# Kernel tuning notes

Measured on AMD Instinct MI355X. Metric: run time of the kernel, lower is better.

Reference implementation:

```python
import jax, jax.numpy as jnp
import numpy as np

N_NODES = 50000
N_EDGES = 800000
IN_FEATS, HIDDEN_FEATS, NUM_CLASSES = 64, 64, 32


def setup_inputs() -> dict:
    key = jax.random.key(0)
    ks = jax.random.split(key, 9)
    features = jax.random.normal(ks[0], (N_NODES, IN_FEATS), dtype=jnp.float32)
    src = jax.random.randint(ks[1], (N_EDGES,), 0, N_NODES, dtype=jnp.int32)
    dst = jax.random.randint(ks[2], (N_EDGES,), 0, N_NODES, dtype=jnp.int32)
    def lin(k, fan_in, fan_out):
        bound = 1.0 / np.sqrt(fan_in)
        return jax.random.uniform(k, (fan_in, fan_out), jnp.float32, -bound, bound)
    W_self1 = lin(ks[3], IN_FEATS, HIDDEN_FEATS)
    W_neigh1 = lin(ks[4], IN_FEATS, HIDDEN_FEATS)
    b1 = jnp.zeros((HIDDEN_FEATS,), jnp.float32)
    W_self2 = lin(ks[5], HIDDEN_FEATS, NUM_CLASSES)
    W_neigh2 = lin(ks[6], HIDDEN_FEATS, NUM_CLASSES)
    b2 = jnp.zeros((NUM_CLASSES,), jnp.float32)
    return {"features": features, "W_self1": W_self1, "W_neigh1": W_neigh1, "b1": b1,
            "W_self2": W_self2, "W_neigh2": W_neigh2, "b2": b2, "src": src, "dst": dst}


def _sage_mean(x, W_self, W_neigh, b, src, dst, n_nodes):
    # mean over in-neighbors: edge (u, v) sends x[u] into v
    agg = jax.ops.segment_sum(x[src], dst, num_segments=n_nodes)          # [N, F]
    deg = jax.ops.segment_sum(jnp.ones((src.shape[0],), x.dtype), dst,
                              num_segments=n_nodes)                        # [N]
    h_neigh = agg / jnp.maximum(deg, 1.0)[:, None]                         # zero-in-degree -> 0
    return x @ W_self + h_neigh @ W_neigh + b


def reference(features, W_self1, W_neigh1, b1, W_self2, W_neigh2, b2, src, dst):
    n = features.shape[0]
    h = jax.nn.relu(_sage_mean(features, W_self1, W_neigh1, b1, src, dst, n))
    return _sage_mean(h, W_self2, W_neigh2, b2, src, dst, n)
```

## Files before the change

### kernel.cpp

```cpp
#include <hip/hip_runtime.h>

#define N_NODES 50000
#define N_EDGES 800000
#define NB 196
#define PBLOCKS 256
#define CHUNK 3125
#define GEMM_BLOCKS 782
#define CSR_CAP 4608
#define HST 80

typedef unsigned short ushort_t;
typedef __attribute__((ext_vector_type(8))) short bf16x8;
typedef __attribute__((ext_vector_type(4))) float f32x4;


__device__ __forceinline__ float bflo(unsigned int u) {
    return __uint_as_float(u << 16);
}
__device__ __forceinline__ float bfhi(unsigned int u) {
    return __uint_as_float(u & 0xffff0000u);
}
__device__ __forceinline__ ushort_t f2bf(float f) {
    unsigned int x = __float_as_uint(f);
    return (ushort_t)((x + 0x7fffu + ((x >> 16) & 1u)) >> 16);
}
__device__ __forceinline__ unsigned int pack_bf(float lo, float hi) {
    return (unsigned int)f2bf(lo) | ((unsigned int)f2bf(hi) << 16);
}
__device__ __forceinline__ void split_bf(float v, short& hi, short& lo) {
    ushort_t h = f2bf(v);
    float r = v - __uint_as_float((unsigned int)h << 16);
    hi = (short)h;
    lo = (short)f2bf(r);
}

__global__ __launch_bounds__(256)
void gemm128_and_count(const float* __restrict__ A,
                       const float* __restrict__ B1,
                       const float* __restrict__ B2,
                       ushort_t* __restrict__ Cself,
                       ushort_t* __restrict__ Cn,
                       const int* __restrict__ dst,
                       int* __restrict__ blocktot) {
    __shared__ int hist[NB];

    if (blockIdx.x >= GEMM_BLOCKS) {
        const int pb = blockIdx.x - GEMM_BLOCKS;
        for (int i = threadIdx.x; i < NB; i += 256) hist[i] = 0;
        __syncthreads();
        const int e0 = pb * CHUNK;
        const int e1 = e0 + CHUNK;
        for (int e = e0 + (int)threadIdx.x; e < e1; e += 256)
            atomicAdd(&hist[dst[e] >> 8], 1);
        __syncthreads();
        for (int i = threadIdx.x; i < NB; i += 256)
            blocktot[i * PBLOCKS + pb] = hist[i];
        return;
    }

    const int l  = threadIdx.x & 63;
    const int w  = threadIdx.x >> 6;
    const int lr = l & 15;
    const int lk = (l >> 4) << 3;

    bf16x8 bhi[2][2], blo[2][2];
#pragma unroll
    for (int nt = 0; nt < 2; ++nt) {
        const int n = w * 32 + nt * 16 + lr;
        const float* Bp = (n < 64) ? (B1 + n) : (B2 + (n - 64));
#pragma unroll
        for (int ks = 0; ks < 2; ++ks) {
#pragma unroll
            for (int j = 0; j < 8; ++j) {
                float bv = Bp[(size_t)(ks * 32 + lk + j) * 64];
                short h, lo;
                split_bf(bv, h, lo);
                bhi[nt][ks][j] = h;
                blo[nt][ks][j] = lo;
            }
        }
    }

    const int m0 = blockIdx.x * 64;
    f32x4 acc[4][2];
#pragma unroll
    for (int mt = 0; mt < 4; ++mt)
#pragma unroll
        for (int nt = 0; nt < 2; ++nt) {
            f32x4 z = {0.f, 0.f, 0.f, 0.f};
            acc[mt][nt] = z;
        }

#pragma unroll
    for (int mt = 0; mt < 4; ++mt) {
        const int m = m0 + mt * 16 + lr;
        const bool valid = (m < N_NODES);
        const float* Ap = A + (size_t)m * 64 + lk;
#pragma unroll
        for (int ks = 0; ks < 2; ++ks) {
            float4 f0, f1;
            if (valid) {
                f0 = *(const float4*)(Ap + ks * 32);
                f1 = *(const float4*)(Ap + ks * 32 + 4);
            } else {
                f0 = make_float4(0.f, 0.f, 0.f, 0.f);
                f1 = f0;
            }
            const float fv[8] = {f0.x, f0.y, f0.z, f0.w, f1.x, f1.y, f1.z, f1.w};
            bf16x8 ahi, alo;
#pragma unroll
            for (int j = 0; j < 8; ++j) {
                short h, lo;
                split_bf(fv[j], h, lo);
                ahi[j] = h;
                alo[j] = lo;
            }
#pragma unroll
            for (int nt = 0; nt < 2; ++nt) {
                acc[mt][nt] = __builtin_amdgcn_mfma_f32_16x16x32_bf16(
                    ahi, bhi[nt][ks], acc[mt][nt], 0, 0, 0);
                acc[mt][nt] = __builtin_amdgcn_mfma_f32_16x16x32_bf16(
                    alo, bhi[nt][ks], acc[mt][nt], 0, 0, 0);
                acc[mt][nt] = __builtin_amdgcn_mfma_f32_16x16x32_bf16(
                    ahi, blo[nt][ks], acc[mt][nt], 0, 0, 0);
            }
        }
    }

#pragma unroll
    for (int mt = 0; mt < 4; ++mt) {
        const int mbase = m0 + mt * 16 + ((l >> 4) << 2);
#pragma unroll
        for (int nt = 0; nt < 2; ++nt) {
            const int n = w * 32 + nt * 16 + lr;
            ushort_t* T = (n < 64) ? (Cself + n) : (Cn + (n - 64));
#pragma unroll
            for (int r = 0; r < 4; ++r) {
                const int m = mbase + r;
                if (m < N_NODES) T[(size_t)m * 64] = f2bf(acc[mt][nt][r]);
            }
        }
    }
}

__global__ __launch_bounds__(256)
void part_write(const int* __restrict__ src, const int* __restrict__ dst,
                const int* __restrict__ blocktot, unsigned int* __restrict__ brec) {
    __shared__ int ssum[256];
    __shared__ int cur[NB];
    const int pb = blockIdx.x;
    const int t  = threadIdx.x;

    int rsum = 0, mypart = 0;
    if (t < NB) {
        const int* rp = blocktot + t * PBLOCKS;
#pragma unroll 8
        for (int j = 0; j < PBLOCKS; ++j) {
            if (j == pb) mypart = rsum;
            rsum += rp[j];
        }
    }
    ssum[t] = (t < NB) ? rsum : 0;
    __syncthreads();
    for (int off = 1; off < 256; off <<= 1) {
        int add = (t >= off) ? ssum[t - off] : 0;
        __syncthreads();
        ssum[t] += add;
        __syncthreads();
    }
    if (t < NB) cur[t] = (ssum[t] - rsum) + mypart;
    __syncthreads();

    const int e0 = pb * CHUNK;
    const int e1 = e0 + CHUNK;
    for (int e = e0 + t; e < e1; e += 256) {
        int d = dst[e];
        int s = src[e];
        int pos = atomicAdd(&cur[d >> 8], 1);
        brec[pos] = ((unsigned int)(d & 255) << 16) | (unsigned int)s;
    }
}

__global__ __launch_bounds__(1024)
void csr_gather1_g2(const int* __restrict__ blocktot,
                    const unsigned int* __restrict__ brec,
                    int* __restrict__ csr_src, int* __restrict__ row_ptr,
                    const ushort_t* __restrict__ Tself,
                    const ushort_t* __restrict__ Tn,
                    const float* __restrict__ bias,
                    const float* __restrict__ Ws2,
                    const float* __restrict__ Wn2,
                    ushort_t* __restrict__ Tself2,
                    ushort_t* __restrict__ Tn2) {
    __shared__ int ssum[256];
    __shared__ int cnt[256];
    __shared__ int rs[256];
    __shared__ int cur[256];
    __shared__ int csr_lds[CSR_CAP];
    __shared__ ushort_t h_lds[256 * HST];

    const int b = blockIdx.x;
    const int node0 = b * 256;
    const int t = threadIdx.x;

    {
        unsigned int* hz = (unsigned int*)h_lds;
        for (int i = t; i < 256 * HST / 2; i += 1024) hz[i] = 0u;
    }

    if (t < 256) {
        int rsum = 0;
        if (t < NB) {
            const int* rp = blocktot + t * PBLOCKS;
#pragma unroll 8
            for (int j = 0; j < PBLOCKS; ++j) rsum += rp[j];
        }
        ssum[t] = rsum;
        cnt[t] = 0;
    }
    __syncthreads();
    for (int off = 1; off < 256; off <<= 1) {
        int add = (t < 256 && t >= off) ? ssum[t - off] : 0;
        __syncthreads();
        if (t < 256) ssum[t] += add;
        __syncthreads();
    }
    const int w0 = (b == 0) ? 0 : ssum[b - 1];
    const int w1 = ssum[b];
    __syncthreads();

    for (int i = w0 + t; i < w1; i += 1024)
        atomicAdd(&cnt[brec[i] >> 16], 1);
    __syncthreads();

    if (t < 256) cur[t] = cnt[t];
    __syncthreads();
    for (int off = 1; off < 256; off <<= 1) {
        int add = (t < 256 && t >= off) ? cur[t - off] : 0;
        __syncthreads();
        if (t < 256) cur[t] += add;
        __syncthreads();
    }
    if (t < 256) {
        const int excl = cur[t] - cnt[t];
        rs[t] = excl;
        const int node = node0 + t;
        if (node <= N_NODES) row_ptr[node] = w0 + excl;
    }
    __syncthreads();
    if (t < 256) cur[t] = rs[t];
    __syncthreads();

    for (int i = w0 + t; i < w1; i += 1024) {
        const unsigned int r = brec[i];
        const int pos = atomicAdd(&cur[r >> 16], 1);
        const int s = (int)(r & 0xffffu);
        csr_src[w0 + pos] = s;
        if (pos < CSR_CAP) csr_lds[pos] = s;
    }
    __syncthreads();

    const int wv   = t >> 6;
    const int lane = t & 63;
    const int half = lane >> 5;
    const int hl   = lane & 31;
    const int r = hl >> 3;
    const int c = hl & 7;

#define ACC8(u)                                           \
    a[0] += bflo(u.x); a[1] += bfhi(u.x);                 \
    a[2] += bflo(u.y); a[3] += bfhi(u.y);                 \
    a[4] += bflo(u.z); a[5] += bfhi(u.z);                 \
    a[6] += bflo(u.w); a[7] += bfhi(u.w);

    for (int it = 0; it < 8; ++it) {
        const int pair = wv + (it << 4);
        const int dloc = (pair << 1) + half;
        const int v = node0 + dloc;
        if (v >= N_NODES) continue;
        const int sl = rs[dloc];
        const int cn = cnt[dloc];

        float a[8];
#pragma unroll
        for (int i = 0; i < 8; ++i) a[i] = 0.f;

        const int nfast = (cn < 32) ? cn : 32;
        int  sidx[8];
        bool act[8];
#pragma unroll
        for (int j = 0; j < 8; ++j) {
            const int tt = r + (j << 2);
            act[j] = (tt < nfast);
            sidx[j] = 0;
            if (act[j]) {
                const int ad = sl + tt;
                sidx[j] = (ad < CSR_CAP) ? csr_lds[ad] : csr_src[w0 + ad];
            }
        }
        uint4 u[8];
#pragma unroll
        for (int j = 0; j < 8; ++j) {
            u[j] = make_uint4(0u, 0u, 0u, 0u);
            if (act[j]) u[j] = *(const uint4*)&Tn[(size_t)sidx[j] * 64 + c * 8];
        }
#pragma unroll
        for (int j = 0; j < 8; ++j) { ACC8(u[j]) }

        for (int tt = 32 + r; tt < cn; tt += 4) {
            const int ad = sl + tt;
            const int s = (ad < CSR_CAP) ? csr_lds[ad] : csr_src[w0 + ad];
            const uint4 uu = *(const uint4*)&Tn[(size_t)s * 64 + c * 8];
            ACC8(uu)
        }

#pragma unroll
        for (int off = 8; off < 32; off <<= 1) {
#pragma unroll
            for (int i = 0; i < 8; ++i) a[i] += __shfl_xor(a[i], off);
        }

        if (r == 0) {
            const float inv = 1.0f / (float)max(cn, 1);
            uint4 su = *(const uint4*)&Tself[(size_t)v * 64 + c * 8];
            float4 bA = *(const float4*)&bias[c * 8];
            float4 bB = *(const float4*)&bias[c * 8 + 4];
            float o[8];
            o[0] = bflo(su.x) + a[0] * inv + bA.x;
            o[1] = bfhi(su.x) + a[1] * inv + bA.y;
            o[2] = bflo(su.y) + a[2] * inv + bA.z;
            o[3] = bfhi(su.y) + a[3] * inv + bA.w;
            o[4] = bflo(su.z) + a[4] * inv + bB.x;
            o[5] = bfhi(su.z) + a[5] * inv + bB.y;
            o[6] = bflo(su.w) + a[6] * inv + bB.z;
            o[7] = bfhi(su.w) + a[7] * inv + bB.w;
#pragma unroll
            for (int i = 0; i < 8; ++i) o[i] = fmaxf(o[i], 0.f);
            uint4 p;
            p.x = pack_bf(o[0], o[1]); p.y = pack_bf(o[2], o[3]);
            p.z = pack_bf(o[4], o[5]); p.w = pack_bf(o[6], o[7]);
            *(uint4*)&h_lds[dloc * HST + c * 8] = p;
        }
    }
#undef ACC8
    __syncthreads();

    const int lr  = lane & 15;
    const int lk2 = (lane >> 4) << 3;

    bf16x8 bhi[4][2], blo[4][2];
#pragma unroll
    for (int nt = 0; nt < 4; ++nt) {
        const int n = nt * 16 + lr;
        const float* Bp = (n < 32) ? (Ws2 + n) : (Wn2 + (n - 32));
#pragma unroll
        for (int ks = 0; ks < 2; ++ks) {
#pragma unroll
            for (int j = 0; j < 8; ++j) {
                float bv = Bp[(size_t)(ks * 32 + lk2 + j) * 32];
                short h, lo;
                split_bf(bv, h, lo);
                bhi[nt][ks][j] = h;
                blo[nt][ks][j] = lo;
            }
        }
    }

    f32x4 acc2[4];
#pragma unroll
    for (int nt = 0; nt < 4; ++nt) {
        f32x4 z = {0.f, 0.f, 0.f, 0.f};
        acc2[nt] = z;
    }
#pragma unroll
    for (int ks = 0; ks < 2; ++ks) {
        const bf16x8 a = *(const bf16x8*)&h_lds[(wv * 16 + lr) * HST + ks * 32 + lk2];
#pragma unroll
        for (int nt = 0; nt < 4; ++nt) {
            acc2[nt] = __builtin_amdgcn_mfma_f32_16x16x32_bf16(a, bhi[nt][ks], acc2[nt], 0, 0, 0);
            acc2[nt] = __builtin_amdgcn_mfma_f32_16x16x32_bf16(a, blo[nt][ks], acc2[nt], 0, 0, 0);
        }
    }

    const int mbase = node0 + wv * 16 + ((lane >> 4) << 2);
#pragma unroll
    for (int nt = 0; nt < 4; ++nt) {
        const int n = nt * 16 + lr;
        ushort_t* T = (n < 32) ? (Tself2 + n) : (Tn2 + (n - 32));
#pragma unroll
        for (int rr = 0; rr < 4; ++rr) {
            const int m = mbase + rr;
            if (m < N_NODES) T[(size_t)m * 32] = f2bf(acc2[nt][rr]);
        }
    }
}

__global__ __launch_bounds__(256)
void gather2(const ushort_t* __restrict__ Tself,
             const ushort_t* __restrict__ Tn,
             const int* __restrict__ row_ptr,
             const int* __restrict__ csr_src, const float* __restrict__ bias,
             float* __restrict__ out) {
    constexpr int F = 32;
    constexpr int LPR = 4;
    constexpr int G = 4;
    constexpr int MAXJ = 8;
    const int lane = threadIdx.x & 63;
    const int q  = lane >> 4;
    const int hl = lane & 15;
    const int r = hl >> 2;
    const int c = hl & 3;
    const int v = (((int)blockIdx.x * (int)blockDim.x + (int)threadIdx.x) >> 6) * 4 + q;
    if (v >= N_NODES) return;
    const int start = row_ptr[v];
    const int cnt   = row_ptr[v + 1] - start;

    float a[8];
#pragma unroll
    for (int i = 0; i < 8; ++i) a[i] = 0.f;

#define ACC8(u)                                           \
    a[0] += bflo(u.x); a[1] += bfhi(u.x);                 \
    a[2] += bflo(u.y); a[3] += bfhi(u.y);                 \
    a[4] += bflo(u.z); a[5] += bfhi(u.z);                 \
    a[6] += bflo(u.w); a[7] += bfhi(u.w);

    int idx0 = 0, idx1 = 0;
    if (hl < cnt)      idx0 = csr_src[start + hl];
    if (16 + hl < cnt) idx1 = csr_src[start + 16 + hl];

    const int nfast = (cnt < 32) ? cnt : 32;
    int  sidx[MAXJ];
    bool act[MAXJ];
#pragma unroll
    for (int j = 0; j < MAXJ; ++j) {
        const int t = r + j * G;
        act[j] = (t < nfast);
        sidx[j] = (j < 4) ? __shfl(idx0, q * 16 + t)
                          : __shfl(idx1, q * 16 + (t - 16));
    }
    uint4 u[MAXJ];
#pragma unroll
    for (int j = 0; j < MAXJ; ++j) {
        u[j] = make_uint4(0u, 0u, 0u, 0u);
        if (act[j]) u[j] = *(const uint4*)&Tn[(size_t)sidx[j] * F + c * 8];
    }
#pragma unroll
    for (int j = 0; j < MAXJ; ++j) { ACC8(u[j]) }

    for (int t = 32 + r; t < cnt; t += G) {
        const int s = csr_src[start + t];
        uint4 uu = *(const uint4*)&Tn[(size_t)s * F + c * 8];
        ACC8(uu)
    }
#undef ACC8

#pragma unroll
    for (int off = LPR; off < 16; off <<= 1) {
#pragma unroll
        for (int i = 0; i < 8; ++i) a[i] += __shfl_xor(a[i], off);
    }

    if (r == 0) {
        const float inv = 1.0f / (float)max(cnt, 1);
        uint4 su = *(const uint4*)&Tself[(size_t)v * F + c * 8];
        float4 bA = *(const float4*)&bias[c * 8];
        float4 bB = *(const float4*)&bias[c * 8 + 4];
        float o[8];
        o[0] = bflo(su.x) + a[0] * inv + bA.x;
        o[1] = bfhi(su.x) + a[1] * inv + bA.y;
        o[2] = bflo(su.y) + a[2] * inv + bA.z;
        o[3] = bfhi(su.y) + a[3] * inv + bA.w;
        o[4] = bflo(su.z) + a[4] * inv + bB.x;
        o[5] = bfhi(su.z) + a[5] * inv + bB.y;
        o[6] = bflo(su.w) + a[6] * inv + bB.z;
        o[7] = bfhi(su.w) + a[7] * inv + bB.w;
        *(float4*)&out[(size_t)v * F + c * 8]     = make_float4(o[0], o[1], o[2], o[3]);
        *(float4*)&out[(size_t)v * F + c * 8 + 4] = make_float4(o[4], o[5], o[6], o[7]);
    }
}

extern "C" void kernel_launch(void* const* d_in, const int* in_sizes, int n_in,
                              void* d_out, int out_size, void* d_ws, size_t ws_size,
                              hipStream_t stream) {
    const float* features = (const float*)d_in[0];
    const float* W_self1  = (const float*)d_in[1];
    const float* W_neigh1 = (const float*)d_in[2];
    const float* b1       = (const float*)d_in[3];
    const float* W_self2  = (const float*)d_in[4];
    const float* W_neigh2 = (const float*)d_in[5];
    const float* b2       = (const float*)d_in[6];
    const int*   src      = (const int*)d_in[7];
    const int*   dst      = (const int*)d_in[8];

    ushort_t* Tself1 = (ushort_t*)d_ws;
    ushort_t* Tn1    = Tself1 + (size_t)N_NODES * 64;
    ushort_t* T2     = Tn1 + (size_t)N_NODES * 64;
    int* row_ptr     = (int*)(T2 + (size_t)N_NODES * 64);
    int* csr_src     = row_ptr + (N_NODES + 1);
    unsigned int* brec = (unsigned int*)(csr_src + N_EDGES);
    int* blocktot    = (int*)(brec + N_EDGES);

    ushort_t* Tself2 = T2;
    ushort_t* Tn2    = T2 + (size_t)N_NODES * 32;

    gemm128_and_count<<<GEMM_BLOCKS + PBLOCKS, 256, 0, stream>>>(
        features, W_self1, W_neigh1, Tself1, Tn1, dst, blocktot);
    part_write<<<PBLOCKS, 256, 0, stream>>>(src, dst, blocktot, brec);
    csr_gather1_g2<<<NB, 1024, 0, stream>>>(
        blocktot, brec, csr_src, row_ptr, Tself1, Tn1, b1,
        W_self2, W_neigh2, Tself2, Tn2);
    gather2<<<(N_NODES + 15) / 16, 256, 0, stream>>>(
        Tself2, Tn2, row_ptr, csr_src, b2, (float*)d_out);
}
```

Baseline: 158.4 us.

## Split CSR-build/gather1 block into two half-blocks of 128 nodes each

The fused CSR-build, layer-1 gather and layer-2 GEMM kernel now launches two 512-thread blocks per 256-node bucket instead of one 1024-thread block. Each half still builds the full bucket histogram and prefix scan, but only scatters, gathers and multiplies the 128 nodes it owns. LDS for the CSR cache and hidden tile shrinks to match. The aim is more blocks (392 vs 196) to fill the GPU's CUs and lower per-block LDS use. The cost is that the counting, scan and brec reads are done twice per bucket.

```diff
diff --git a/kernel.cpp b/kernel.cpp
--- a/kernel.cpp
+++ b/kernel.cpp
@@ -6,7 +6,7 @@
 #define PBLOCKS 256
 #define CHUNK 3125
 #define GEMM_BLOCKS 782
-#define CSR_CAP 4608
+#define CSR_CAP 2560
 #define HST 80
 
 typedef unsigned short ushort_t;
@@ -181,7 +181,7 @@
     }
 }
 
-__global__ __launch_bounds__(1024)
+__global__ __launch_bounds__(512)
 void csr_gather1_g2(const int* __restrict__ blocktot,
                     const unsigned int* __restrict__ brec,
                     int* __restrict__ csr_src, int* __restrict__ row_ptr,
@@ -197,15 +197,16 @@
     __shared__ int rs[256];
     __shared__ int cur[256];
     __shared__ int csr_lds[CSR_CAP];
-    __shared__ ushort_t h_lds[256 * HST];
-
-    const int b = blockIdx.x;
+    __shared__ ushort_t h_lds[128 * HST];
+
+    const int b    = blockIdx.x >> 1;
+    const int half = blockIdx.x & 1;
     const int node0 = b * 256;
     const int t = threadIdx.x;
 
     {
         unsigned int* hz = (unsigned int*)h_lds;
-        for (int i = t; i < 256 * HST / 2; i += 1024) hz[i] = 0u;
+        for (int i = t; i < 128 * HST / 2; i += 512) hz[i] = 0u;
     }
 
     if (t < 256) {
@@ -229,7 +230,7 @@
     const int w1 = ssum[b];
     __syncthreads();
 
-    for (int i = w0 + t; i < w1; i += 1024)
+    for (int i = w0 + t; i < w1; i += 512)
         atomicAdd(&cnt[brec[i] >> 16], 1);
     __syncthreads();
 
@@ -244,25 +245,33 @@
     if (t < 256) {
         const int excl = cur[t] - cnt[t];
         rs[t] = excl;
-        const int node = node0 + t;
-        if (node <= N_NODES) row_ptr[node] = w0 + excl;
+        if ((t >> 7) == half) {
+            const int node = node0 + t;
+            if (node <= N_NODES) row_ptr[node] = w0 + excl;
+        }
     }
     __syncthreads();
     if (t < 256) cur[t] = rs[t];
     __syncthreads();
 
-    for (int i = w0 + t; i < w1; i += 1024) {
+    const int lbase = rs[half * 128];
+
+    for (int i = w0 + t; i < w1; i += 512) {
         const unsigned int r = brec[i];
-        const int pos = atomicAdd(&cur[r >> 16], 1);
-        const int s = (int)(r & 0xffffu);
-        csr_src[w0 + pos] = s;
-        if (pos < CSR_CAP) csr_lds[pos] = s;
+        const int dloc = (int)(r >> 16);
+        if ((dloc >> 7) == half) {
+            const int pos = atomicAdd(&cur[dloc], 1);
+            const int s = (int)(r & 0xffffu);
+            csr_src[w0 + pos] = s;
+            const int lp = pos - lbase;
+            if (lp < CSR_CAP) csr_lds[lp] = s;
+        }
     }
     __syncthreads();
 
     const int wv   = t >> 6;
     const int lane = t & 63;
-    const int half = lane >> 5;
+    const int lh   = lane >> 5;
     const int hl   = lane & 31;
     const int r = hl >> 3;
     const int c = hl & 7;
@@ -274,8 +283,8 @@
     a[6] += bflo(u.w); a[7] += bfhi(u.w);
 
     for (int it = 0; it < 8; ++it) {
-        const int pair = wv + (it << 4);
-        const int dloc = (pair << 1) + half;
+        const int dll = (((wv + (it << 3)) << 1) + lh);
+        const int dloc = half * 128 + dll;
         const int v = node0 + dloc;
         if (v >= N_NODES) continue;
         const int sl = rs[dloc];
@@ -295,7 +304,8 @@
             sidx[j] = 0;
             if (act[j]) {
                 const int ad = sl + tt;
-                sidx[j] = (ad < CSR_CAP) ? csr_lds[ad] : csr_src[w0 + ad];
+                const int lp = ad - lbase;
+                sidx[j] = (lp < CSR_CAP) ? csr_lds[lp] : csr_src[w0 + ad];
             }
         }
         uint4 u[8];
@@ -309,7 +319,8 @@
 
         for (int tt = 32 + r; tt < cn; tt += 4) {
             const int ad = sl + tt;
-            const int s = (ad < CSR_CAP) ? csr_lds[ad] : csr_src[w0 + ad];
+            const int lp = ad - lbase;
+            const int s = (lp < CSR_CAP) ? csr_lds[lp] : csr_src[w0 + ad];
             const uint4 uu = *(const uint4*)&Tn[(size_t)s * 64 + c * 8];
             ACC8(uu)
         }
@@ -339,7 +350,7 @@
             uint4 p;
             p.x = pack_bf(o[0], o[1]); p.y = pack_bf(o[2], o[3]);
             p.z = pack_bf(o[4], o[5]); p.w = pack_bf(o[6], o[7]);
-            *(uint4*)&h_lds[dloc * HST + c * 8] = p;
+            *(uint4*)&h_lds[dll * HST + c * 8] = p;
         }
     }
 #undef ACC8
@@ -382,7 +393,7 @@
         }
     }
 
-    const int mbase = node0 + wv * 16 + ((lane >> 4) << 2);
+    const int mbase = node0 + half * 128 + wv * 16 + ((lane >> 4) << 2);
 #pragma unroll
     for (int nt = 0; nt < 4; ++nt) {
         const int n = nt * 16 + lr;
@@ -507,7 +518,7 @@
     gemm128_and_count<<<GEMM_BLOCKS + PBLOCKS, 256, 0, stream>>>(
         features, W_self1, W_neigh1, Tself1, Tn1, dst, blocktot);
     part_write<<<PBLOCKS, 256, 0, stream>>>(src, dst, blocktot, brec);
-    csr_gather1_g2<<<NB, 1024, 0, stream>>>(
+    csr_gather1_g2<<<NB * 2, 512, 0, stream>>>(
         blocktot, brec, csr_src, row_ptr, Tself1, Tn1, b1,
         W_self2, W_neigh2, Tself2, Tn2);
     gather2<<<(N_NODES + 15) / 16, 256, 0, stream>>>(
```

After: 169.6 us. 7.1% more time.

## Shrink CSR buckets to 64 nodes and precompute bucket starts in partition pass

Applied to the files above, without the earlier changes.

Bucket granularity for the edge partition goes from 256 nodes to 64 nodes, so the fused CSR build and layer-1 gather runs as 782 blocks of 256 threads instead of 196 blocks of 1024. Each gather block now handles fewer nodes and needs much less shared memory, which should allow more blocks per CU and better load balance. The global bucket prefix sum moves into part_write, which is now 1024-thread, and is written once to a bucketstart array, so gather blocks no longer rescan blocktot. The cost is a larger blocktot histogram and a 1024-wide scan in every partition block.

```diff
diff --git a/kernel.cpp b/kernel.cpp
--- a/kernel.cpp
+++ b/kernel.cpp
@@ -2,11 +2,11 @@
 
 #define N_NODES 50000
 #define N_EDGES 800000
-#define NB 196
+#define NB 782
 #define PBLOCKS 256
 #define CHUNK 3125
 #define GEMM_BLOCKS 782
-#define CSR_CAP 4608
+#define CSR_CAP 1536
 #define HST 80
 
 typedef unsigned short ushort_t;
@@ -51,10 +51,10 @@
         const int e0 = pb * CHUNK;
         const int e1 = e0 + CHUNK;
         for (int e = e0 + (int)threadIdx.x; e < e1; e += 256)
-            atomicAdd(&hist[dst[e] >> 8], 1);
+            atomicAdd(&hist[dst[e] >> 6], 1);
         __syncthreads();
         for (int i = threadIdx.x; i < NB; i += 256)
-            blocktot[i * PBLOCKS + pb] = hist[i];
+            blocktot[pb * NB + i] = hist[i];
         return;
     }
 
@@ -143,47 +143,52 @@
     }
 }
 
-__global__ __launch_bounds__(256)
+__global__ __launch_bounds__(1024)
 void part_write(const int* __restrict__ src, const int* __restrict__ dst,
-                const int* __restrict__ blocktot, unsigned int* __restrict__ brec) {
-    __shared__ int ssum[256];
+                const int* __restrict__ blocktot, unsigned int* __restrict__ brec,
+                int* __restrict__ bucketstart) {
+    __shared__ int psum[1024];
     __shared__ int cur[NB];
     const int pb = blockIdx.x;
     const int t  = threadIdx.x;
 
     int rsum = 0, mypart = 0;
     if (t < NB) {
-        const int* rp = blocktot + t * PBLOCKS;
 #pragma unroll 8
         for (int j = 0; j < PBLOCKS; ++j) {
             if (j == pb) mypart = rsum;
-            rsum += rp[j];
-        }
-    }
-    ssum[t] = (t < NB) ? rsum : 0;
-    __syncthreads();
-    for (int off = 1; off < 256; off <<= 1) {
-        int add = (t >= off) ? ssum[t - off] : 0;
-        __syncthreads();
-        ssum[t] += add;
-        __syncthreads();
-    }
-    if (t < NB) cur[t] = (ssum[t] - rsum) + mypart;
+            rsum += blocktot[j * NB + t];
+        }
+    }
+    psum[t] = rsum;
+    __syncthreads();
+    for (int off = 1; off < 1024; off <<= 1) {
+        int add = (t >= off) ? psum[t - off] : 0;
+        __syncthreads();
+        psum[t] += add;
+        __syncthreads();
+    }
+    if (t < NB) {
+        const int rowpre = psum[t] - rsum;
+        cur[t] = rowpre + mypart;
+        if (pb == 0) bucketstart[t] = rowpre;
+    }
+    if (pb == 0 && t == 0) bucketstart[NB] = N_EDGES;
     __syncthreads();
 
     const int e0 = pb * CHUNK;
     const int e1 = e0 + CHUNK;
-    for (int e = e0 + t; e < e1; e += 256) {
+    for (int e = e0 + t; e < e1; e += 1024) {
         int d = dst[e];
         int s = src[e];
-        int pos = atomicAdd(&cur[d >> 8], 1);
-        brec[pos] = ((unsigned int)(d & 255) << 16) | (unsigned int)s;
-    }
-}
-
-__global__ __launch_bounds__(1024)
-void csr_gather1_g2(const int* __restrict__ blocktot,
-                    const unsigned int* __restrict__ brec,
+        int pos = atomicAdd(&cur[d >> 6], 1);
+        brec[pos] = ((unsigned int)(d & 63) << 16) | (unsigned int)s;
+    }
+}
+
+__global__ __launch_bounds__(256)
+void csr_gather1_g2(const unsigned int* __restrict__ brec,
+                    const int* __restrict__ bucketstart,
                     int* __restrict__ csr_src, int* __restrict__ row_ptr,
                     const ushort_t* __restrict__ Tself,
                     const ushort_t* __restrict__ Tn,
@@ -192,66 +197,43 @@
                     const float* __restrict__ Wn2,
                     ushort_t* __restrict__ Tself2,
                     ushort_t* __restrict__ Tn2) {
-    __shared__ int ssum[256];
-    __shared__ int cnt[256];
-    __shared__ int rs[256];
-    __shared__ int cur[256];
+    __shared__ int cnt[64];
+    __shared__ int rs[64];
+    __shared__ int cur[64];
     __shared__ int csr_lds[CSR_CAP];
-    __shared__ ushort_t h_lds[256 * HST];
+    __shared__ ushort_t h_lds[64 * HST];
 
     const int b = blockIdx.x;
-    const int node0 = b * 256;
+    const int node0 = b * 64;
     const int t = threadIdx.x;
-
-    {
-        unsigned int* hz = (unsigned int*)h_lds;
-        for (int i = t; i < 256 * HST / 2; i += 1024) hz[i] = 0u;
-    }
-
-    if (t < 256) {
-        int rsum = 0;
-        if (t < NB) {
-            const int* rp = blocktot + t * PBLOCKS;
-#pragma unroll 8
-            for (int j = 0; j < PBLOCKS; ++j) rsum += rp[j];
-        }
-        ssum[t] = rsum;
-        cnt[t] = 0;
-    }
-    __syncthreads();
-    for (int off = 1; off < 256; off <<= 1) {
-        int add = (t < 256 && t >= off) ? ssum[t - off] : 0;
-        __syncthreads();
-        if (t < 256) ssum[t] += add;
-        __syncthreads();
-    }
-    const int w0 = (b == 0) ? 0 : ssum[b - 1];
-    const int w1 = ssum[b];
-    __syncthreads();
-
-    for (int i = w0 + t; i < w1; i += 1024)
+    const int w0 = bucketstart[b];
+    const int w1 = bucketstart[b + 1];
+
+    if (t < 64) cnt[t] = 0;
+    __syncthreads();
+
+    for (int i = w0 + t; i < w1; i += 256)
         atomicAdd(&cnt[brec[i] >> 16], 1);
     __syncthreads();
 
-    if (t < 256) cur[t] = cnt[t];
-    __syncthreads();
-    for (int off = 1; off < 256; off <<= 1) {
-        int add = (t < 256 && t >= off) ? cur[t - off] : 0;
-        __syncthreads();
-        if (t < 256) cur[t] += add;
-        __syncthreads();
-    }
-    if (t < 256) {
+    if (t < 64) cur[t] = cnt[t];
+    __syncthreads();
+    for (int off = 1; off < 64; off <<= 1) {
+        int add = (t < 64 && t >= off) ? cur[t - off] : 0;
+        __syncthreads();
+        if (t < 64) cur[t] += add;
+        __syncthreads();
+    }
+    if (t < 64) {
         const int excl = cur[t] - cnt[t];
         rs[t] = excl;
         const int node = node0 + t;
         if (node <= N_NODES) row_ptr[node] = w0 + excl;
-    }
-    __syncthreads();
-    if (t < 256) cur[t] = rs[t];
-    __syncthreads();
-
-    for (int i = w0 + t; i < w1; i += 1024) {
+        cur[t] = excl;
+    }
+    __syncthreads();
+
+    for (int i = w0 + t; i < w1; i += 256) {
         const unsigned int r = brec[i];
         const int pos = atomicAdd(&cur[r >> 16], 1);
         const int s = (int)(r & 0xffffu);
@@ -262,7 +244,7 @@
 
     const int wv   = t >> 6;
     const int lane = t & 63;
-    const int half = lane >> 5;
+    const int lh   = lane >> 5;
     const int hl   = lane & 31;
     const int r = hl >> 3;
     const int c = hl & 7;
@@ -274,8 +256,7 @@
     a[6] += bflo(u.w); a[7] += bfhi(u.w);
 
     for (int it = 0; it < 8; ++it) {
-        const int pair = wv + (it << 4);
-        const int dloc = (pair << 1) + half;
+        const int dloc = (((wv + (it << 2)) << 1) + lh);
         const int v = node0 + dloc;
         if (v >= N_NODES) continue;
         const int sl = rs[dloc];
@@ -500,15 +481,16 @@
     int* csr_src     = row_ptr + (N_NODES + 1);
     unsigned int* brec = (unsigned int*)(csr_src + N_EDGES);
     int* blocktot    = (int*)(brec + N_EDGES);
+    int* bucketstart = blocktot + PBLOCKS * NB;
 
     ushort_t* Tself2 = T2;
     ushort_t* Tn2    = T2 + (size_t)N_NODES * 32;
 
     gemm128_and_count<<<GEMM_BLOCKS + PBLOCKS, 256, 0, stream>>>(
         features, W_self1, W_neigh1, Tself1, Tn1, dst, blocktot);
-    part_write<<<PBLOCKS, 256, 0, stream>>>(src, dst, blocktot, brec);
-    csr_gather1_g2<<<NB, 1024, 0, stream>>>(
-        blocktot, brec, csr_src, row_ptr, Tself1, Tn1, b1,
+    part_write<<<PBLOCKS, 1024, 0, stream>>>(src, dst, blocktot, brec, bucketstart);
+    csr_gather1_g2<<<NB, 256, 0, stream>>>(
+        brec, bucketstart, csr_src, row_ptr, Tself1, Tn1, b1,
         W_self2, W_neigh2, Tself2, Tn2);
     gather2<<<(N_NODES + 15) / 16, 256, 0, stream>>>(
         Tself2, Tn2, row_ptr, csr_src, b2, (float*)d_out);
```

Result: slower. 183.6 us (+15.9%).
